# Kernel tuning notes

Hardware: AMD Instinct MI355X
Metric: run time of the kernel (lower is better)

Reference implementation:

```python
import jax, jax.numpy as jnp
import numpy as np

N, E, C, H = 50000, 800000, 64, 64
EPS = 1e-5


def _edge_conv(x, src, dst, Wa, ba, Wb, bb):
    # PyG EdgeConv: h_i = max_{j in N(i)} MLP([x_i, x_j - x_i]), aggr='max'
    xi = x[dst]                      # [E, C] target features
    xj = x[src]                      # [E, C] source features
    h = jnp.concatenate([xi, xj - xi], axis=-1)   # [E, 2C]
    h = jax.nn.relu(h @ Wa + ba)
    h = jax.nn.relu(h @ Wb + bb)     # [E, H]
    out = jax.ops.segment_max(h, dst, num_segments=x.shape[0])
    # nodes with no incoming edge: segment_max yields -inf -> fill with 0
    return jnp.where(jnp.isneginf(out), 0.0, out)


def _batchnorm(x, gamma, beta):
    # training-mode BatchNorm1d: biased batch stats over the node dim
    mean = jnp.mean(x, axis=0)
    var = jnp.var(x, axis=0)
    return gamma * (x - mean) * jax.lax.rsqrt(var + EPS) + beta


def setup_inputs() -> dict:
    key = jax.random.key(0)
    ks = jax.random.split(key, 12)
    x = jax.random.normal(ks[0], (N, C), dtype=jnp.float32)
    edge_index = jax.random.randint(ks[1], (2, E), 0, N, dtype=jnp.int64)
    batch = jnp.zeros((N,), dtype=jnp.int64)
    s1 = 1.0 / np.sqrt(2 * C)
    s2 = 1.0 / np.sqrt(H)
    return {
        "x": x,
        "edge_index": edge_index,
        "batch": batch,
        "W1a": jax.random.normal(ks[2], (2 * C, H), jnp.float32) * s1,
        "b1a": jnp.zeros((H,), jnp.float32),
        "W1b": jax.random.normal(ks[3], (H, H), jnp.float32) * s2,
        "b1b": jnp.zeros((H,), jnp.float32),
        "gamma1": jnp.ones((H,), jnp.float32),
        "beta1": jnp.zeros((H,), jnp.float32),
        "W2a": jax.random.normal(ks[4], (2 * H, H), jnp.float32) * s2,
        "b2a": jnp.zeros((H,), jnp.float32),
        "W2b": jax.random.normal(ks[5], (H, H), jnp.float32) * s2,
        "b2b": jnp.zeros((H,), jnp.float32),
        "gamma2": jnp.ones((H,), jnp.float32),
        "beta2": jnp.zeros((H,), jnp.float32),
    }


def reference(x, edge_index, batch, W1a, b1a, W1b, b1b, gamma1, beta1,
              W2a, b2a, W2b, b2b, gamma2, beta2):
    src, dst = edge_index[0], edge_index[1]
    h = _edge_conv(x, src, dst, W1a, b1a, W1b, b1b)
    h = _batchnorm(h, gamma1, beta1)
    h = _edge_conv(h, src, dst, W2a, b2a, W2b, b2b)
    h = _batchnorm(h, gamma2, beta2)
    return h
```

## Files before the change

kernel.cpp:

```cpp
#include <hip/hip_runtime.h>
#include <hip/hip_bf16.h>

typedef float f32x4 __attribute__((ext_vector_type(4)));
typedef short s16x8 __attribute__((ext_vector_type(8)));

#define EPS 1e-5f

__device__ __forceinline__ unsigned short f32_to_bf16_rne(float f) {
    unsigned u = __float_as_uint(f);
    unsigned r = u + 0x7FFFu + ((u >> 16) & 1u);
    return (unsigned short)(r >> 16);
}

__device__ __forceinline__ unsigned cvtpk(float a, float b) {
    unsigned d;
    asm("v_cvt_pk_bf16_f32 %0, %1, %2" : "=v"(d) : "v"(a), "v"(b));
    return d;
}

#define DPPF(v, c) __int_as_float(__builtin_amdgcn_update_dpp(0, __float_as_int(v), (c), 0xF, 0xF, true))
#define SWZ4(v) __int_as_float(__builtin_amdgcn_ds_swizzle(__float_as_int(v), 0x101F))

__global__ void pack_zero(const float* __restrict__ W1a, const float* __restrict__ W1b,
                          const float* __restrict__ W2b, unsigned short* __restrict__ p,
                          float* __restrict__ stats, int* __restrict__ count, int N) {
    int idx = blockIdx.x * 256 + threadIdx.x;
    if (idx < 16384) {
        int m = idx >> 12;
        int t = idx & 4095;
        int j = t & 7;
        int lane = (t >> 3) & 63;
        int mt = (t >> 9) & 3;
        int kc = t >> 11;
        int k = kc * 32 + (lane >> 4) * 8 + j;
        int c = mt * 16 + (lane & 15);
        float v;
        int dst;
        switch (m) {
            case 0: v = W1a[k * 64 + c] - W1a[(k + 64) * 64 + c]; dst = t; break;
            case 1: v = W1a[(k + 64) * 64 + c]; dst = 4096 + t; break;
            case 2: v = W1b[k * 64 + c]; dst = 8192 + t; break;
            default: v = W2b[k * 64 + c]; dst = 20480 + t; break;
        }
        p[dst] = f32_to_bf16_rne(v);
    } else if (idx < 16640) {
        stats[idx - 16384] = 0.f;
    } else if (idx - 16640 < N) {
        count[idx - 16640] = 0;
    }
}

__global__ void cvt_hist(const float* __restrict__ in, unsigned short* __restrict__ out, int n4,
                         const int* __restrict__ edst, int* __restrict__ count, int E) {
    int i = blockIdx.x * 256 + threadIdx.x;
    if (i < n4) {
        f32x4 v = ((const f32x4*)in)[i];
        uint2 pr;
        pr.x = cvtpk(v[0], v[1]);
        pr.y = cvtpk(v[2], v[3]);
        *(uint2*)(out + i * 4) = pr;
    }
    if (i < E) atomicAdd(&count[edst[i]], 1);
}

__global__ void scan1(const int* __restrict__ count, int* __restrict__ offsets,
                      int* __restrict__ bsums, int N) {
    __shared__ int sdata[256];
    int t = threadIdx.x;
    int base = blockIdx.x * 1024 + t * 4;
    int4 v = {0, 0, 0, 0};
    if (base + 3 < N) {
        v = *(const int4*)(count + base);
    } else {
        if (base + 0 < N) v.x = count[base + 0];
        if (base + 1 < N) v.y = count[base + 1];
        if (base + 2 < N) v.z = count[base + 2];
    }
    int s = v.x + v.y + v.z + v.w;
    sdata[t] = s;
    __syncthreads();
    for (int off = 1; off < 256; off <<= 1) {
        int u = (t >= off) ? sdata[t - off] : 0;
        __syncthreads();
        sdata[t] += u;
        __syncthreads();
    }
    int excl = sdata[t] - s;
    if (t == 255) bsums[blockIdx.x] = sdata[255];
    int o0 = excl;
    int o1 = o0 + v.x;
    int o2 = o1 + v.y;
    int o3 = o2 + v.z;
    if (base + 0 < N) offsets[base + 0] = o0;
    if (base + 1 < N) offsets[base + 1] = o1;
    if (base + 2 < N) offsets[base + 2] = o2;
    if (base + 3 < N) offsets[base + 3] = o3;
}

__global__ void scan2(int* __restrict__ bsums, int* __restrict__ offsets, int N, int nb) {
    __shared__ int sdata[256];
    int t = threadIdx.x;
    int s = (t < nb) ? bsums[t] : 0;
    sdata[t] = s;
    __syncthreads();
    for (int off = 1; off < 256; off <<= 1) {
        int u = (t >= off) ? sdata[t - off] : 0;
        __syncthreads();
        sdata[t] += u;
        __syncthreads();
    }
    if (t < nb) bsums[t] = sdata[t] - s;
    if (t == 255) offsets[N] = sdata[255];
}

__global__ void scan3(int* __restrict__ offsets, int* __restrict__ cursor,
                      const int* __restrict__ bsums, int N) {
    int i = blockIdx.x * 256 + threadIdx.x;
    if (i < N) {
        int v = offsets[i] + bsums[i >> 10];
        offsets[i] = v;
        cursor[i] = v;
    }
}

__global__ void scatter_kernel(const int* __restrict__ esrc, const int* __restrict__ edst,
                               int* __restrict__ cursor, int* __restrict__ ssrc, int E) {
    int i = blockIdx.x * 256 + threadIdx.x;
    if (i < E) {
        int d = edst[i];
        int pos = atomicAdd(&cursor[d], 1);
        ssrc[pos] = esrc[i];
    }
}

__global__ void repack2(const float* __restrict__ stats, const float* __restrict__ gamma1,
                        const float* __restrict__ beta1, const float* __restrict__ W2a,
                        const float* __restrict__ b2a, unsigned short* __restrict__ pw2,
                        float* __restrict__ b2adj, float invN) {
    __shared__ float sc[64], sh[64];
    __shared__ float part[4][64];
    int tid = threadIdx.x;
    if (tid < 64) {
        float mean = stats[tid] * invN;
        float var = stats[64 + tid] * invN - mean * mean;
        float s = gamma1[tid] * rsqrtf(var + EPS);
        sc[tid] = s;
        sh[tid] = beta1[tid] - mean * s;
    }
    __syncthreads();
    if (blockIdx.x == 0) {
        int c = tid & 63, sl = tid >> 6;
        float a = 0.f;
#pragma unroll
        for (int kk = 0; kk < 16; ++kk) {
            int k = sl * 16 + kk;
            a += sh[k] * W2a[k * 64 + c];
        }
        part[sl][c] = a;
        __syncthreads();
        if (tid < 64)
            b2adj[tid] = b2a[tid] + part[0][tid] + part[1][tid] + part[2][tid] + part[3][tid];
    }

    for (int e = blockIdx.x * 256 + tid; e < 8192; e += 16 * 256) {
        int m = e >> 12;
        int t = e & 4095;
        int j = t & 7;
        int lane = (t >> 3) & 63;
        int mt = (t >> 9) & 3;
        int kc = t >> 11;
        int k = kc * 32 + (lane >> 4) * 8 + j;
        int c = mt * 16 + (lane & 15);
        float wtop = W2a[k * 64 + c];
        float wbot = W2a[(k + 64) * 64 + c];
        float v = (m == 0) ? sc[k] * (wtop - wbot) : sc[k] * wbot;
        pw2[e] = f32_to_bf16_rne(v);
    }
}

#define LSTR 72
__global__ __launch_bounds__(256, 4) void edgeconv_sorted(
    const unsigned short* __restrict__ xb,
    const int* __restrict__ ssrc,
    const int* __restrict__ offsets,
    const unsigned short* __restrict__ pW,
    const float* __restrict__ ba,
    const float* __restrict__ bb,
    float* __restrict__ outf,
    unsigned short* __restrict__ outb,
    float* __restrict__ statsOut,
    int N) {
    __shared__ __align__(16) unsigned short lw[12288];
    __shared__ __align__(16) unsigned short xh[4][16 * LSTR];
    __shared__ float sred[128];
    const int tid = threadIdx.x;
    const int w = tid >> 6;
    const int lane = tid & 63;
    const int g = lane >> 4;
    const int r = lane & 15;
    const int srow = lane >> 2;
    const int schk = lane & 3;

    for (int i = tid; i < 1536; i += 256)
        ((s16x8*)lw)[i] = ((const s16x8*)pW)[i];
    if (tid < 128) sred[tid] = 0.f;
    __syncthreads();

    const unsigned short* wxi = lw;
    const unsigned short* wxj = lw + 4096;
    const unsigned short* wb = lw + 8192;

    unsigned short* myb = xh[w];
    const int totalWaves = gridDim.x * 4;
    const f32x4 zf = {0.f, 0.f, 0.f, 0.f};

    const int ch = (r >> 2) * 16 + g * 4 + (r & 3);
    const float b2l = bb[ch];
    float bsum = 0.f, bss = 0.f;

    for (int node = blockIdx.x * 4 + w; node < N; node += totalWaves) {
        const int segB = offsets[node];
        const int segE = offsets[node + 1];

        f32x4 rm[4];
#pragma unroll
        for (int mt = 0; mt < 4; ++mt)
            rm[mt] = (f32x4){-INFINITY, -INFINITY, -INFINITY, -INFINITY};

        if (segB < segE) {
            int sv = ssrc[min(segB + srow, segE - 1)];
            s16x8 ra = *(const s16x8*)(xb + sv * 64 + schk * 8);
            s16x8 rb = *(const s16x8*)(xb + sv * 64 + 32 + schk * 8);

            s16x8 xi1 = *(const s16x8*)(xb + node * 64 + g * 8);
            s16x8 xi2 = *(const s16x8*)(xb + node * 64 + 32 + g * 8);
            f32x4 accxi[4];
#pragma unroll
            for (int mt = 0; mt < 4; ++mt)
                accxi[mt] = *(const f32x4*)(ba + mt * 16 + g * 4);
#pragma unroll
            for (int mt = 0; mt < 4; ++mt) {
                s16x8 f0 = *(const s16x8*)(wxi + ((0 * 4 + mt) * 64 + lane) * 8);
                accxi[mt] = __builtin_amdgcn_mfma_f32_16x16x32_bf16(f0, xi1, accxi[mt], 0, 0, 0);
                s16x8 f1 = *(const s16x8*)(wxi + ((1 * 4 + mt) * 64 + lane) * 8);
                accxi[mt] = __builtin_amdgcn_mfma_f32_16x16x32_bf16(f1, xi2, accxi[mt], 0, 0, 0);
            }

            for (int t0 = segB; t0 < segE; t0 += 16) {
                *(s16x8*)(myb + srow * LSTR + schk * 8) = ra;
                *(s16x8*)(myb + srow * LSTR + 32 + schk * 8) = rb;
                s16x8 xj1 = *(const s16x8*)(myb + r * LSTR + g * 8);
                s16x8 xj2 = *(const s16x8*)(myb + r * LSTR + 32 + g * 8);

                int t1 = t0 + 16;
                if (t1 < segE) {
                    int sv2 = ssrc[min(t1 + srow, segE - 1)];
                    ra = *(const s16x8*)(xb + sv2 * 64 + schk * 8);
                    rb = *(const s16x8*)(xb + sv2 * 64 + 32 + schk * 8);
                }

                f32x4 acc[4];
#pragma unroll
                for (int mt = 0; mt < 4; ++mt) {
                    s16x8 a0 = *(const s16x8*)(wxj + ((0 * 4 + mt) * 64 + lane) * 8);
                    acc[mt] = __builtin_amdgcn_mfma_f32_16x16x32_bf16(a0, xj1, accxi[mt], 0, 0, 0);
                    s16x8 a1 = *(const s16x8*)(wxj + ((1 * 4 + mt) * 64 + lane) * 8);
                    acc[mt] = __builtin_amdgcn_mfma_f32_16x16x32_bf16(a1, xj2, acc[mt], 0, 0, 0);
                }

#pragma unroll
                for (int mt = 0; mt < 4; ++mt) {
                    uint2 pr;
                    pr.x = cvtpk(fmaxf(acc[mt][0], 0.f), fmaxf(acc[mt][1], 0.f));
                    pr.y = cvtpk(fmaxf(acc[mt][2], 0.f), fmaxf(acc[mt][3], 0.f));
                    *(uint2*)(myb + r * LSTR + mt * 16 + g * 4) = pr;
                }
                s16x8 p0 = *(const s16x8*)(myb + r * LSTR + g * 8);
                s16x8 p1 = *(const s16x8*)(myb + r * LSTR + 32 + g * 8);

                f32x4 acc2[4];
#pragma unroll
                for (int mt = 0; mt < 4; ++mt) {
                    s16x8 b0 = *(const s16x8*)(wb + ((0 * 4 + mt) * 64 + lane) * 8);
                    acc2[mt] = __builtin_amdgcn_mfma_f32_16x16x32_bf16(b0, p0, zf, 0, 0, 0);
                    s16x8 b1 = *(const s16x8*)(wb + ((1 * 4 + mt) * 64 + lane) * 8);
                    acc2[mt] = __builtin_amdgcn_mfma_f32_16x16x32_bf16(b1, p1, acc2[mt], 0, 0, 0);
                }

#pragma unroll
                for (int mt = 0; mt < 4; ++mt)
#pragma unroll
                    for (int q = 0; q < 4; ++q)
                        rm[mt][q] = fmaxf(rm[mt][q], acc2[mt][q]);
            }
        }

        float k8[8];
#pragma unroll
        for (int j = 0; j < 8; ++j) {
            float lo = rm[j >> 2][j & 3];
            float hv = rm[(j >> 2) + 2][j & 3];
            float tlo = DPPF(lo, 0x128);
            float thi = DPPF(hv, 0x128);
            float own = (r & 8) ? hv : lo;
            float oth = (r & 8) ? thi : tlo;
            k8[j] = fmaxf(own, oth);
        }
        float k4[4];
#pragma unroll
        for (int j = 0; j < 4; ++j) {
            float ta = SWZ4(k8[j]);
            float tb = SWZ4(k8[j + 4]);
            float own = (r & 4) ? k8[j + 4] : k8[j];
            float oth = (r & 4) ? tb : ta;
            k4[j] = fmaxf(own, oth);
        }
        float k2[2];
#pragma unroll
        for (int j = 0; j < 2; ++j) {
            float ta = DPPF(k4[j], 0x4E);
            float tb = DPPF(k4[j + 2], 0x4E);
            float own = (r & 2) ? k4[j + 2] : k4[j];
            float oth = (r & 2) ? tb : ta;
            k2[j] = fmaxf(own, oth);
        }
        float ta = DPPF(k2[0], 0xB1);
        float tb = DPPF(k2[1], 0xB1);
        float vfin = fmaxf((r & 1) ? k2[1] : k2[0], (r & 1) ? tb : ta);

        float o = fmaxf(vfin + b2l, 0.f);
        if (outb)
            outb[node * 64 + ch] = f32_to_bf16_rne(o);
        else
            outf[node * 64 + ch] = o;
        bsum += o;
        bss += o * o;
    }

    atomicAdd(&sred[ch], bsum);
    atomicAdd(&sred[64 + ch], bss);
    __syncthreads();
    if (tid < 128) atomicAdd(&statsOut[tid], sred[tid]);
}

__global__ void bn_apply(const float* __restrict__ in, const float* __restrict__ stats,
                         const float* __restrict__ gamma, const float* __restrict__ beta,
                         float* __restrict__ outf, int n4, float invN) {
    int i = blockIdx.x * 256 + threadIdx.x;
    if (i >= n4) return;
    int c0 = (i * 4) & 63;
    f32x4 v = ((const f32x4*)in)[i];
    f32x4 o;
#pragma unroll
    for (int q = 0; q < 4; ++q) {
        int c = c0 + q;
        float mean = stats[c] * invN;
        float var = stats[64 + c] * invN - mean * mean;
        float sc = gamma[c] * rsqrtf(var + EPS);
        o[q] = (v[q] - mean) * sc + beta[c];
    }
    ((f32x4*)outf)[i] = o;
}

extern "C" void kernel_launch(void* const* d_in, const int* in_sizes, int n_in,
                              void* d_out, int out_size, void* d_ws, size_t ws_size,
                              hipStream_t stream) {
    const float* x = (const float*)d_in[0];
    const int* ei = (const int*)d_in[1];
    const float* W1a = (const float*)d_in[3];
    const float* b1a = (const float*)d_in[4];
    const float* W1b = (const float*)d_in[5];
    const float* b1b = (const float*)d_in[6];
    const float* gamma1 = (const float*)d_in[7];
    const float* beta1 = (const float*)d_in[8];
    const float* W2a = (const float*)d_in[9];
    const float* b2a = (const float*)d_in[10];
    const float* W2b = (const float*)d_in[11];
    const float* b2b = (const float*)d_in[12];
    const float* gamma2 = (const float*)d_in[13];
    const float* beta2 = (const float*)d_in[14];

    const int N = in_sizes[0] / 64;
    const int E = in_sizes[1] / 2;
    const int NC = N * 64;

    char* ws = (char*)d_ws;
    size_t off = 0;
    auto alloc = [&](size_t bytes) {
        char* p = ws + off;
        off += (bytes + 255) & ~(size_t)255;
        return p;
    };
    unsigned short* xb1 = (unsigned short*)alloc((size_t)NC * 2);
    unsigned short* xb2 = (unsigned short*)alloc((size_t)NC * 2);
    unsigned short* pw = (unsigned short*)alloc(24576 * 2);
    float* stats = (float*)alloc(256 * 4);
    float* b2adj = (float*)alloc(64 * 4);
    int* count = (int*)alloc((size_t)N * 4);
    int* offsets = (int*)alloc((size_t)(N + 1) * 4);
    int* cursor = (int*)alloc((size_t)(N + 1) * 4);
    int* ssrc = (int*)alloc((size_t)E * 4);
    int* bsums = (int*)alloc(1024 * 4);

    const int* esrc = ei;
    const int* edst = ei + E;

    int pgrid = (16640 + N + 255) / 256;
    pack_zero<<<pgrid, 256, 0, stream>>>(W1a, W1b, W2b, pw, stats, count, N);

    int n4 = NC / 4;
    int big = max(n4, E);
    cvt_hist<<<(big + 255) / 256, 256, 0, stream>>>(x, xb1, n4, edst, count, E);

    int nb = (N + 1023) / 1024;
    scan1<<<nb, 256, 0, stream>>>(count, offsets, bsums, N);
    scan2<<<1, 256, 0, stream>>>(bsums, offsets, N, nb);
    scan3<<<(N + 255) / 256, 256, 0, stream>>>(offsets, cursor, bsums, N);
    scatter_kernel<<<(E + 255) / 256, 256, 0, stream>>>(esrc, edst, cursor, ssrc, E);

    const int egrid = 2048;

    edgeconv_sorted<<<egrid, 256, 0, stream>>>(xb1, ssrc, offsets, pw, b1a, b1b,
                                               nullptr, xb2, stats, N);

    repack2<<<16, 256, 0, stream>>>(stats, gamma1, beta1, W2a, b2a, pw + 12288, b2adj, 1.0f / N);

    edgeconv_sorted<<<egrid, 256, 0, stream>>>(xb2, ssrc, offsets, pw + 12288, b2adj, b2b,
                                               (float*)d_out, nullptr, stats + 128, N);

    int cgrid = (n4 + 255) / 256;
    bn_apply<<<cgrid, 256, 0, stream>>>((float*)d_out, stats + 128, gamma2, beta2,
                                        (float*)d_out, n4, 1.0f / N);
}
```

Before: 247.4 us.

## Process two destination nodes per wave to interleave independent MFMA chains

Each wave now handles two nodes at once (nA and nA+totalWaves). It runs both edge-tile MLP chains in lockstep with separate LDS staging buffers, so independent MFMA and gather latency can overlap. This aims to raise instruction-level parallelism in the gather-MLP-max loop. In exchange it doubles register and LDS use, lowers launch-bounds occupancy from 4 to 3, and wastes work when the two nodes have different edge counts, since the loop runs to the larger tile count with clamped indices.

```diff
diff --git a/kernel.cpp b/kernel.cpp
--- a/kernel.cpp
+++ b/kernel.cpp
@@ -179,7 +179,7 @@
 }
 
 #define LSTR 72
-__global__ __launch_bounds__(256, 4) void edgeconv_sorted(
+__global__ __launch_bounds__(256, 3) void edgeconv_sorted(
     const unsigned short* __restrict__ xb,
     const int* __restrict__ ssrc,
     const int* __restrict__ offsets,
@@ -191,7 +191,7 @@
     float* __restrict__ statsOut,
     int N) {
     __shared__ __align__(16) unsigned short lw[12288];
-    __shared__ __align__(16) unsigned short xh[4][16 * LSTR];
+    __shared__ __align__(16) unsigned short xh[4][2 * 16 * LSTR];
     __shared__ float sred[128];
     const int tid = threadIdx.x;
     const int w = tid >> 6;
@@ -210,131 +210,190 @@
     const unsigned short* wxj = lw + 4096;
     const unsigned short* wb = lw + 8192;
 
-    unsigned short* myb = xh[w];
+    unsigned short* mybA = xh[w];
+    unsigned short* mybB = xh[w] + 16 * LSTR;
     const int totalWaves = gridDim.x * 4;
+    const int stride2 = totalWaves * 2;
     const f32x4 zf = {0.f, 0.f, 0.f, 0.f};
 
     const int ch = (r >> 2) * 16 + g * 4 + (r & 3);
     const float b2l = bb[ch];
     float bsum = 0.f, bss = 0.f;
 
-    for (int node = blockIdx.x * 4 + w; node < N; node += totalWaves) {
-        const int segB = offsets[node];
-        const int segE = offsets[node + 1];
-
-        f32x4 rm[4];
+    for (int nA = blockIdx.x * 4 + w; nA < N; nA += stride2) {
+        const int nB = nA + totalWaves;
+        const bool hasB = nB < N;
+        const int rowB = hasB ? nB : nA;
+
+        const int sBA = offsets[nA];
+        const int sEA = offsets[nA + 1];
+        int sBB = sBA, sEB = sEA;
+        if (hasB) {
+            sBB = offsets[nB];
+            sEB = offsets[nB + 1];
+        }
+        const bool vA = sEA > sBA;
+        const bool vB = hasB && (sEB > sBB);
+        const int ntA = vA ? (sEA - sBA + 15) >> 4 : 1;
+        const int ntB = vB ? (sEB - sBB + 15) >> 4 : 1;
+        const int nt = max(ntA, ntB);
+
+        int ivA = max(min(sBA + srow, sEA - 1), 0);
+        int ivB = max(min(sBB + srow, sEB - 1), 0);
+        int svA = ssrc[ivA];
+        int svB = ssrc[ivB];
+        s16x8 raA = *(const s16x8*)(xb + svA * 64 + schk * 8);
+        s16x8 rbA = *(const s16x8*)(xb + svA * 64 + 32 + schk * 8);
+        s16x8 raB = *(const s16x8*)(xb + svB * 64 + schk * 8);
+        s16x8 rbB = *(const s16x8*)(xb + svB * 64 + 32 + schk * 8);
+
+        s16x8 xiA1 = *(const s16x8*)(xb + nA * 64 + g * 8);
+        s16x8 xiA2 = *(const s16x8*)(xb + nA * 64 + 32 + g * 8);
+        s16x8 xiB1 = *(const s16x8*)(xb + rowB * 64 + g * 8);
+        s16x8 xiB2 = *(const s16x8*)(xb + rowB * 64 + 32 + g * 8);
+        f32x4 accxiA[4], accxiB[4];
+#pragma unroll
+        for (int mt = 0; mt < 4; ++mt) {
+            f32x4 bias = *(const f32x4*)(ba + mt * 16 + g * 4);
+            s16x8 f0 = *(const s16x8*)(wxi + ((0 * 4 + mt) * 64 + lane) * 8);
+            s16x8 f1 = *(const s16x8*)(wxi + ((1 * 4 + mt) * 64 + lane) * 8);
+            f32x4 cA = __builtin_amdgcn_mfma_f32_16x16x32_bf16(f0, xiA1, bias, 0, 0, 0);
+            f32x4 cB = __builtin_amdgcn_mfma_f32_16x16x32_bf16(f0, xiB1, bias, 0, 0, 0);
+            accxiA[mt] = __builtin_amdgcn_mfma_f32_16x16x32_bf16(f1, xiA2, cA, 0, 0, 0);
+            accxiB[mt] = __builtin_amdgcn_mfma_f32_16x16x32_bf16(f1, xiB2, cB, 0, 0, 0);
+        }
+
+        f32x4 rmA[4], rmB[4];
+#pragma unroll
+        for (int mt = 0; mt < 4; ++mt) {
+            rmA[mt] = (f32x4){-INFINITY, -INFINITY, -INFINITY, -INFINITY};
+            rmB[mt] = (f32x4){-INFINITY, -INFINITY, -INFINITY, -INFINITY};
+        }
+
+        for (int it = 0; it < nt; ++it) {
+            *(s16x8*)(mybA + srow * LSTR + schk * 8) = raA;
+            *(s16x8*)(mybA + srow * LSTR + 32 + schk * 8) = rbA;
+            *(s16x8*)(mybB + srow * LSTR + schk * 8) = raB;
+            *(s16x8*)(mybB + srow * LSTR + 32 + schk * 8) = rbB;
+            s16x8 xjA1 = *(const s16x8*)(mybA + r * LSTR + g * 8);
+            s16x8 xjA2 = *(const s16x8*)(mybA + r * LSTR + 32 + g * 8);
+            s16x8 xjB1 = *(const s16x8*)(mybB + r * LSTR + g * 8);
+            s16x8 xjB2 = *(const s16x8*)(mybB + r * LSTR + 32 + g * 8);
+
+            if (it + 1 < nt) {
+                int tA2 = sBA + 16 * min(it + 1, ntA - 1);
+                int tB2 = sBB + 16 * min(it + 1, ntB - 1);
+                int iA2 = max(min(tA2 + srow, sEA - 1), 0);
+                int iB2 = max(min(tB2 + srow, sEB - 1), 0);
+                svA = ssrc[iA2];
+                svB = ssrc[iB2];
+                raA = *(const s16x8*)(xb + svA * 64 + schk * 8);
+                rbA = *(const s16x8*)(xb + svA * 64 + 32 + schk * 8);
+                raB = *(const s16x8*)(xb + svB * 64 + schk * 8);
+                rbB = *(const s16x8*)(xb + svB * 64 + 32 + schk * 8);
+            }
+
+            f32x4 accA[4], accB[4];
+#pragma unroll
+            for (int mt = 0; mt < 4; ++mt) {
+                s16x8 a0 = *(const s16x8*)(wxj + ((0 * 4 + mt) * 64 + lane) * 8);
+                accA[mt] = __builtin_amdgcn_mfma_f32_16x16x32_bf16(a0, xjA1, accxiA[mt], 0, 0, 0);
+                accB[mt] = __builtin_amdgcn_mfma_f32_16x16x32_bf16(a0, xjB1, accxiB[mt], 0, 0, 0);
+                s16x8 a1 = *(const s16x8*)(wxj + ((1 * 4 + mt) * 64 + lane) * 8);
+                accA[mt] = __builtin_amdgcn_mfma_f32_16x16x32_bf16(a1, xjA2, accA[mt], 0, 0, 0);
+                accB[mt] = __builtin_amdgcn_mfma_f32_16x16x32_bf16(a1, xjB2, accB[mt], 0, 0, 0);
+            }
+
+#pragma unroll
+            for (int mt = 0; mt < 4; ++mt) {
+                uint2 prA, prB;
+                prA.x = cvtpk(fmaxf(accA[mt][0], 0.f), fmaxf(accA[mt][1], 0.f));
+                prA.y = cvtpk(fmaxf(accA[mt][2], 0.f), fmaxf(accA[mt][3], 0.f));
+                *(uint2*)(mybA + r * LSTR + mt * 16 + g * 4) = prA;
+                prB.x = cvtpk(fmaxf(accB[mt][0], 0.f), fmaxf(accB[mt][1], 0.f));
+                prB.y = cvtpk(fmaxf(accB[mt][2], 0.f), fmaxf(accB[mt][3], 0.f));
+                *(uint2*)(mybB + r * LSTR + mt * 16 + g * 4) = prB;
+            }
+            s16x8 pA0 = *(const s16x8*)(mybA + r * LSTR + g * 8);
+            s16x8 pA1 = *(const s16x8*)(mybA + r * LSTR + 32 + g * 8);
+            s16x8 pB0 = *(const s16x8*)(mybB + r * LSTR + g * 8);
+            s16x8 pB1 = *(const s16x8*)(mybB + r * LSTR + 32 + g * 8);
+
+            f32x4 acc2A[4], acc2B[4];
+#pragma unroll
+            for (int mt = 0; mt < 4; ++mt) {
+                s16x8 b0 = *(const s16x8*)(wb + ((0 * 4 + mt) * 64 + lane) * 8);
+                acc2A[mt] = __builtin_amdgcn_mfma_f32_16x16x32_bf16(b0, pA0, zf, 0, 0, 0);
+                acc2B[mt] = __builtin_amdgcn_mfma_f32_16x16x32_bf16(b0, pB0, zf, 0, 0, 0);
+                s16x8 b1 = *(const s16x8*)(wb + ((1 * 4 + mt) * 64 + lane) * 8);
+                acc2A[mt] = __builtin_amdgcn_mfma_f32_16x16x32_bf16(b1, pA1, acc2A[mt], 0, 0, 0);
+                acc2B[mt] = __builtin_amdgcn_mfma_f32_16x16x32_bf16(b1, pB1, acc2B[mt], 0, 0, 0);
+            }
+
+#pragma unroll
+            for (int mt = 0; mt < 4; ++mt)
+#pragma unroll
+                for (int q = 0; q < 4; ++q) {
+                    rmA[mt][q] = fmaxf(rmA[mt][q], acc2A[mt][q]);
+                    rmB[mt][q] = fmaxf(rmB[mt][q], acc2B[mt][q]);
+                }
+        }
+
 #pragma unroll
         for (int mt = 0; mt < 4; ++mt)
-            rm[mt] = (f32x4){-INFINITY, -INFINITY, -INFINITY, -INFINITY};
-
-        if (segB < segE) {
-            int sv = ssrc[min(segB + srow, segE - 1)];
-            s16x8 ra = *(const s16x8*)(xb + sv * 64 + schk * 8);
-            s16x8 rb = *(const s16x8*)(xb + sv * 64 + 32 + schk * 8);
-
-            s16x8 xi1 = *(const s16x8*)(xb + node * 64 + g * 8);
-            s16x8 xi2 = *(const s16x8*)(xb + node * 64 + 32 + g * 8);
-            f32x4 accxi[4];
-#pragma unroll
-            for (int mt = 0; mt < 4; ++mt)
-                accxi[mt] = *(const f32x4*)(ba + mt * 16 + g * 4);
-#pragma unroll
-            for (int mt = 0; mt < 4; ++mt) {
-                s16x8 f0 = *(const s16x8*)(wxi + ((0 * 4 + mt) * 64 + lane) * 8);
-                accxi[mt] = __builtin_amdgcn_mfma_f32_16x16x32_bf16(f0, xi1, accxi[mt], 0, 0, 0);
-                s16x8 f1 = *(const s16x8*)(wxi + ((1 * 4 + mt) * 64 + lane) * 8);
-                accxi[mt] = __builtin_amdgcn_mfma_f32_16x16x32_bf16(f1, xi2, accxi[mt], 0, 0, 0);
-            }
-
-            for (int t0 = segB; t0 < segE; t0 += 16) {
-                *(s16x8*)(myb + srow * LSTR + schk * 8) = ra;
-                *(s16x8*)(myb + srow * LSTR + 32 + schk * 8) = rb;
-                s16x8 xj1 = *(const s16x8*)(myb + r * LSTR + g * 8);
-                s16x8 xj2 = *(const s16x8*)(myb + r * LSTR + 32 + g * 8);
-
-                int t1 = t0 + 16;
-                if (t1 < segE) {
-                    int sv2 = ssrc[min(t1 + srow, segE - 1)];
-                    ra = *(const s16x8*)(xb + sv2 * 64 + schk * 8);
-                    rb = *(const s16x8*)(xb + sv2 * 64 + 32 + schk * 8);
-                }
-
-                f32x4 acc[4];
-#pragma unroll
-                for (int mt = 0; mt < 4; ++mt) {
-                    s16x8 a0 = *(const s16x8*)(wxj + ((0 * 4 + mt) * 64 + lane) * 8);
-                    acc[mt] = __builtin_amdgcn_mfma_f32_16x16x32_bf16(a0, xj1, accxi[mt], 0, 0, 0);
-                    s16x8 a1 = *(const s16x8*)(wxj + ((1 * 4 + mt) * 64 + lane) * 8);
-                    acc[mt] = __builtin_amdgcn_mfma_f32_16x16x32_bf16(a1, xj2, acc[mt], 0, 0, 0);
-                }
-
-#pragma unroll
-                for (int mt = 0; mt < 4; ++mt) {
-                    uint2 pr;
-                    pr.x = cvtpk(fmaxf(acc[mt][0], 0.f), fmaxf(acc[mt][1], 0.f));
-                    pr.y = cvtpk(fmaxf(acc[mt][2], 0.f), fmaxf(acc[mt][3], 0.f));
-                    *(uint2*)(myb + r * LSTR + mt * 16 + g * 4) = pr;
-                }
-                s16x8 p0 = *(const s16x8*)(myb + r * LSTR + g * 8);
-                s16x8 p1 = *(const s16x8*)(myb + r * LSTR + 32 + g * 8);
-
-                f32x4 acc2[4];
-#pragma unroll
-                for (int mt = 0; mt < 4; ++mt) {
-                    s16x8 b0 = *(const s16x8*)(wb + ((0 * 4 + mt) * 64 + lane) * 8);
-                    acc2[mt] = __builtin_amdgcn_mfma_f32_16x16x32_bf16(b0, p0, zf, 0, 0, 0);
-                    s16x8 b1 = *(const s16x8*)(wb + ((1 * 4 + mt) * 64 + lane) * 8);
-                    acc2[mt] = __builtin_amdgcn_mfma_f32_16x16x32_bf16(b1, p1, acc2[mt], 0, 0, 0);
-                }
-
-#pragma unroll
-                for (int mt = 0; mt < 4; ++mt)
-#pragma unroll
-                    for (int q = 0; q < 4; ++q)
-                        rm[mt][q] = fmaxf(rm[mt][q], acc2[mt][q]);
-            }
-        }
-
-        float k8[8];
-#pragma unroll
-        for (int j = 0; j < 8; ++j) {
-            float lo = rm[j >> 2][j & 3];
-            float hv = rm[(j >> 2) + 2][j & 3];
-            float tlo = DPPF(lo, 0x128);
-            float thi = DPPF(hv, 0x128);
-            float own = (r & 8) ? hv : lo;
-            float oth = (r & 8) ? thi : tlo;
-            k8[j] = fmaxf(own, oth);
-        }
-        float k4[4];
-#pragma unroll
-        for (int j = 0; j < 4; ++j) {
-            float ta = SWZ4(k8[j]);
-            float tb = SWZ4(k8[j + 4]);
-            float own = (r & 4) ? k8[j + 4] : k8[j];
-            float oth = (r & 4) ? tb : ta;
-            k4[j] = fmaxf(own, oth);
-        }
-        float k2[2];
-#pragma unroll
-        for (int j = 0; j < 2; ++j) {
-            float ta = DPPF(k4[j], 0x4E);
-            float tb = DPPF(k4[j + 2], 0x4E);
-            float own = (r & 2) ? k4[j + 2] : k4[j];
-            float oth = (r & 2) ? tb : ta;
-            k2[j] = fmaxf(own, oth);
-        }
-        float ta = DPPF(k2[0], 0xB1);
-        float tb = DPPF(k2[1], 0xB1);
-        float vfin = fmaxf((r & 1) ? k2[1] : k2[0], (r & 1) ? tb : ta);
-
-        float o = fmaxf(vfin + b2l, 0.f);
-        if (outb)
-            outb[node * 64 + ch] = f32_to_bf16_rne(o);
-        else
-            outf[node * 64 + ch] = o;
-        bsum += o;
-        bss += o * o;
+#pragma unroll
+            for (int q = 0; q < 4; ++q) {
+                rmA[mt][q] = vA ? rmA[mt][q] : -INFINITY;
+                rmB[mt][q] = vB ? rmB[mt][q] : -INFINITY;
+            }
+
+#pragma unroll
+        for (int nsel = 0; nsel < 2; ++nsel) {
+            const f32x4* rm = nsel ? rmB : rmA;
+            float k8[8];
+#pragma unroll
+            for (int j = 0; j < 8; ++j) {
+                float lo = rm[j >> 2][j & 3];
+                float hv = rm[(j >> 2) + 2][j & 3];
+                float tlo = DPPF(lo, 0x128);
+                float thi = DPPF(hv, 0x128);
+                float own = (r & 8) ? hv : lo;
+                float oth = (r & 8) ? thi : tlo;
+                k8[j] = fmaxf(own, oth);
+            }
+            float k4[4];
+#pragma unroll
+            for (int j = 0; j < 4; ++j) {
+                float ta = SWZ4(k8[j]);
+                float tb = SWZ4(k8[j + 4]);
+                float own = (r & 4) ? k8[j + 4] : k8[j];
+                float oth = (r & 4) ? tb : ta;
+                k4[j] = fmaxf(own, oth);
+            }
+            float k2[2];
+#pragma unroll
+            for (int j = 0; j < 2; ++j) {
+                float ta = DPPF(k4[j], 0x4E);
+                float tb = DPPF(k4[j + 2], 0x4E);
+                float own = (r & 2) ? k4[j + 2] : k4[j];
+                float oth = (r & 2) ? tb : ta;
+                k2[j] = fmaxf(own, oth);
+            }
+            float ta = DPPF(k2[0], 0xB1);
+            float tb = DPPF(k2[1], 0xB1);
+            float vfin = fmaxf((r & 1) ? k2[1] : k2[0], (r & 1) ? tb : ta);
+
+            float o = fmaxf(vfin + b2l, 0.f);
+            int node = nsel ? nB : nA;
+            if (!nsel || hasB) {
+                if (outb)
+                    outb[node * 64 + ch] = f32_to_bf16_rne(o);
+                else
+                    outf[node * 64 + ch] = o;
+                bsum += o;
+                bss += o * o;
+            }
+        }
     }
 
     atomicAdd(&sred[ch], bsum);
```

Result: slower. 354.5 us (+43.3%).

## Drop scan3 pass by folding block offsets into consumers; keep Wb in registers

Applied to the files above, without the earlier changes.

Removes the third scan kernel: scan1 writes block-local offsets into both offsets and cursor, and scatter and edgeconv add the per-block prefix from bsums when they read them. This saves one kernel launch and one pass over the offsets array, at the cost of an extra bsums lookup per edge and per node. In addition, the second-layer weight fragments (Wb) are loaded once into registers per wave instead of being read from LDS on every edge tile. That cuts LDS reads and LDS footprint but adds register pressure under the 256-thread, 4-block launch bound.

```diff
diff --git a/kernel.cpp b/kernel.cpp
--- a/kernel.cpp
+++ b/kernel.cpp
@@ -64,7 +64,7 @@
 }
 
 __global__ void scan1(const int* __restrict__ count, int* __restrict__ offsets,
-                      int* __restrict__ bsums, int N) {
+                      int* __restrict__ cursor, int* __restrict__ bsums, int N) {
     __shared__ int sdata[256];
     int t = threadIdx.x;
     int base = blockIdx.x * 1024 + t * 4;
@@ -91,10 +91,10 @@
     int o1 = o0 + v.x;
     int o2 = o1 + v.y;
     int o3 = o2 + v.z;
-    if (base + 0 < N) offsets[base + 0] = o0;
-    if (base + 1 < N) offsets[base + 1] = o1;
-    if (base + 2 < N) offsets[base + 2] = o2;
-    if (base + 3 < N) offsets[base + 3] = o3;
+    if (base + 0 < N) { offsets[base + 0] = o0; cursor[base + 0] = o0; }
+    if (base + 1 < N) { offsets[base + 1] = o1; cursor[base + 1] = o1; }
+    if (base + 2 < N) { offsets[base + 2] = o2; cursor[base + 2] = o2; }
+    if (base + 3 < N) { offsets[base + 3] = o3; cursor[base + 3] = o3; }
 }
 
 __global__ void scan2(int* __restrict__ bsums, int* __restrict__ offsets, int N, int nb) {
@@ -113,22 +113,13 @@
     if (t == 255) offsets[N] = sdata[255];
 }
 
-__global__ void scan3(int* __restrict__ offsets, int* __restrict__ cursor,
-                      const int* __restrict__ bsums, int N) {
-    int i = blockIdx.x * 256 + threadIdx.x;
-    if (i < N) {
-        int v = offsets[i] + bsums[i >> 10];
-        offsets[i] = v;
-        cursor[i] = v;
-    }
-}
-
 __global__ void scatter_kernel(const int* __restrict__ esrc, const int* __restrict__ edst,
-                               int* __restrict__ cursor, int* __restrict__ ssrc, int E) {
+                               int* __restrict__ cursor, const int* __restrict__ bsums,
+                               int* __restrict__ ssrc, int E) {
     int i = blockIdx.x * 256 + threadIdx.x;
     if (i < E) {
         int d = edst[i];
-        int pos = atomicAdd(&cursor[d], 1);
+        int pos = atomicAdd(&cursor[d], 1) + bsums[d >> 10];
         ssrc[pos] = esrc[i];
     }
 }
@@ -183,14 +174,16 @@
     const unsigned short* __restrict__ xb,
     const int* __restrict__ ssrc,
     const int* __restrict__ offsets,
-    const unsigned short* __restrict__ pW,
+    const int* __restrict__ bsums,
+    const unsigned short* __restrict__ pWab,
+    const unsigned short* __restrict__ pWb,
     const float* __restrict__ ba,
     const float* __restrict__ bb,
     float* __restrict__ outf,
     unsigned short* __restrict__ outb,
     float* __restrict__ statsOut,
     int N) {
-    __shared__ __align__(16) unsigned short lw[12288];
+    __shared__ __align__(16) unsigned short lw[8192];
     __shared__ __align__(16) unsigned short xh[4][16 * LSTR];
     __shared__ float sred[128];
     const int tid = threadIdx.x;
@@ -201,14 +194,20 @@
     const int srow = lane >> 2;
     const int schk = lane & 3;
 
-    for (int i = tid; i < 1536; i += 256)
-        ((s16x8*)lw)[i] = ((const s16x8*)pW)[i];
+    for (int i = tid; i < 1024; i += 256)
+        ((s16x8*)lw)[i] = ((const s16x8*)pWab)[i];
     if (tid < 128) sred[tid] = 0.f;
+
+    s16x8 ab[2][4];
+#pragma unroll
+    for (int kc = 0; kc < 2; ++kc)
+#pragma unroll
+        for (int mt = 0; mt < 4; ++mt)
+            ab[kc][mt] = *(const s16x8*)(pWb + ((kc * 4 + mt) * 64 + lane) * 8);
     __syncthreads();
 
     const unsigned short* wxi = lw;
     const unsigned short* wxj = lw + 4096;
-    const unsigned short* wb = lw + 8192;
 
     unsigned short* myb = xh[w];
     const int totalWaves = gridDim.x * 4;
@@ -219,8 +218,9 @@
     float bsum = 0.f, bss = 0.f;
 
     for (int node = blockIdx.x * 4 + w; node < N; node += totalWaves) {
-        const int segB = offsets[node];
-        const int segE = offsets[node + 1];
+        const int segB = offsets[node] + bsums[node >> 10];
+        const int np1 = node + 1;
+        const int segE = offsets[np1] + ((np1 < N) ? bsums[np1 >> 10] : 0);
 
         f32x4 rm[4];
 #pragma unroll
@@ -281,10 +281,8 @@
                 f32x4 acc2[4];
 #pragma unroll
                 for (int mt = 0; mt < 4; ++mt) {
-                    s16x8 b0 = *(const s16x8*)(wb + ((0 * 4 + mt) * 64 + lane) * 8);
-                    acc2[mt] = __builtin_amdgcn_mfma_f32_16x16x32_bf16(b0, p0, zf, 0, 0, 0);
-                    s16x8 b1 = *(const s16x8*)(wb + ((1 * 4 + mt) * 64 + lane) * 8);
-                    acc2[mt] = __builtin_amdgcn_mfma_f32_16x16x32_bf16(b1, p1, acc2[mt], 0, 0, 0);
+                    acc2[mt] = __builtin_amdgcn_mfma_f32_16x16x32_bf16(ab[0][mt], p0, zf, 0, 0, 0);
+                    acc2[mt] = __builtin_amdgcn_mfma_f32_16x16x32_bf16(ab[1][mt], p1, acc2[mt], 0, 0, 0);
                 }
 
 #pragma unroll
@@ -413,20 +411,19 @@
     cvt_hist<<<(big + 255) / 256, 256, 0, stream>>>(x, xb1, n4, edst, count, E);
 
     int nb = (N + 1023) / 1024;
-    scan1<<<nb, 256, 0, stream>>>(count, offsets, bsums, N);
+    scan1<<<nb, 256, 0, stream>>>(count, offsets, cursor, bsums, N);
     scan2<<<1, 256, 0, stream>>>(bsums, offsets, N, nb);
-    scan3<<<(N + 255) / 256, 256, 0, stream>>>(offsets, cursor, bsums, N);
-    scatter_kernel<<<(E + 255) / 256, 256, 0, stream>>>(esrc, edst, cursor, ssrc, E);
+    scatter_kernel<<<(E + 255) / 256, 256, 0, stream>>>(esrc, edst, cursor, bsums, ssrc, E);
 
     const int egrid = 2048;
 
-    edgeconv_sorted<<<egrid, 256, 0, stream>>>(xb1, ssrc, offsets, pw, b1a, b1b,
-                                               nullptr, xb2, stats, N);
+    edgeconv_sorted<<<egrid, 256, 0, stream>>>(xb1, ssrc, offsets, bsums, pw, pw + 8192,
+                                               b1a, b1b, nullptr, xb2, stats, N);
 
     repack2<<<16, 256, 0, stream>>>(stats, gamma1, beta1, W2a, b2a, pw + 12288, b2adj, 1.0f / N);
 
-    edgeconv_sorted<<<egrid, 256, 0, stream>>>(xb2, ssrc, offsets, pw + 12288, b2adj, b2b,
-                                               (float*)d_out, nullptr, stats + 128, N);
+    edgeconv_sorted<<<egrid, 256, 0, stream>>>(xb2, ssrc, offsets, bsums, pw + 12288, pw + 20480,
+                                               b2adj, b2b, (float*)d_out, nullptr, stats + 128, N);
 
     int cgrid = (n4 + 255) / 256;
     bn_apply<<<cgrid, 256, 0, stream>>>((float*)d_out, stats + 128, gamma2, beta2,
```

Result: slower. 298.4 us (+20.6%).
